# Optimization experiments

Hardware: AMD Instinct MI355X
Metric: run time of the kernel (lower is better)

## Reference

```python
import jax, jax.numpy as jnp
import numpy as np

NUM_SHOT = 1024
D_MODEL = 512
NHEAD = 8
NLAYERS = 6
D_FF = 2048
EPS = 1e-5


def _ln(x, s, b):
    m = jnp.mean(x, axis=-1, keepdims=True)
    v = jnp.mean(jnp.square(x - m), axis=-1, keepdims=True)
    return (x - m) / jnp.sqrt(v + EPS) * s + b


def _mha(q_in, kv_in, w_qkv, b_qkv, w_o, b_o):
    # q_in: [Sq, D], kv_in: [Sk, D]; PyTorch in_proj layout [3D, D]
    D = q_in.shape[-1]
    hd = D // NHEAD
    wq, wk, wv = w_qkv[:D], w_qkv[D:2 * D], w_qkv[2 * D:]
    bq, bk, bv = b_qkv[:D], b_qkv[D:2 * D], b_qkv[2 * D:]
    q = (q_in @ wq.T + bq).reshape(-1, NHEAD, hd)
    k = (kv_in @ wk.T + bk).reshape(-1, NHEAD, hd)
    v = (kv_in @ wv.T + bv).reshape(-1, NHEAD, hd)
    scores = jnp.einsum('qhd,khd->hqk', q, k) * (1.0 / np.sqrt(hd))
    a = jax.nn.softmax(scores, axis=-1)
    o = jnp.einsum('hqk,khd->qhd', a, v).reshape(-1, D)
    return o @ w_o.T + b_o


def setup_inputs() -> dict:
    key = jax.random.key(0)
    ks = iter(jax.random.split(key, 40))
    L, D, F = NLAYERS, D_MODEL, D_FF
    SC = 0.05  # weight scale, keeps activations sane

    def w(shape):
        return jax.random.normal(next(ks), shape, dtype=jnp.float32) * SC

    inp = {'shot_feature': jax.random.normal(next(ks), (NUM_SHOT, D), dtype=jnp.float32)}
    inp.update(
        enc_qkv_w=w((L, 3 * D, D)), enc_qkv_b=jnp.zeros((L, 3 * D), jnp.float32),
        enc_out_w=w((L, D, D)), enc_out_b=jnp.zeros((L, D), jnp.float32),
        enc_ff1_w=w((L, F, D)), enc_ff1_b=jnp.zeros((L, F), jnp.float32),
        enc_ff2_w=w((L, D, F)), enc_ff2_b=jnp.zeros((L, D), jnp.float32),
        enc_ln1_s=jnp.ones((L, D), jnp.float32), enc_ln1_b=jnp.zeros((L, D), jnp.float32),
        enc_ln2_s=jnp.ones((L, D), jnp.float32), enc_ln2_b=jnp.zeros((L, D), jnp.float32),
        dec_sa_qkv_w=w((L, 3 * D, D)), dec_sa_qkv_b=jnp.zeros((L, 3 * D), jnp.float32),
        dec_sa_out_w=w((L, D, D)), dec_sa_out_b=jnp.zeros((L, D), jnp.float32),
        dec_ca_qkv_w=w((L, 3 * D, D)), dec_ca_qkv_b=jnp.zeros((L, 3 * D), jnp.float32),
        dec_ca_out_w=w((L, D, D)), dec_ca_out_b=jnp.zeros((L, D), jnp.float32),
        dec_ff1_w=w((L, F, D)), dec_ff1_b=jnp.zeros((L, F), jnp.float32),
        dec_ff2_w=w((L, D, F)), dec_ff2_b=jnp.zeros((L, D), jnp.float32),
        dec_ln1_s=jnp.ones((L, D), jnp.float32), dec_ln1_b=jnp.zeros((L, D), jnp.float32),
        dec_ln2_s=jnp.ones((L, D), jnp.float32), dec_ln2_b=jnp.zeros((L, D), jnp.float32),
        dec_ln3_s=jnp.ones((L, D), jnp.float32), dec_ln3_b=jnp.zeros((L, D), jnp.float32),
        enc_norm_s=jnp.ones((D,), jnp.float32), enc_norm_b=jnp.zeros((D,), jnp.float32),
        dec_norm_s=jnp.ones((D,), jnp.float32), dec_norm_b=jnp.zeros((D,), jnp.float32),
    )
    return inp


def reference(shot_feature, enc_qkv_w, enc_qkv_b, enc_out_w, enc_out_b,
              enc_ff1_w, enc_ff1_b, enc_ff2_w, enc_ff2_b,
              enc_ln1_s, enc_ln1_b, enc_ln2_s, enc_ln2_b,
              dec_sa_qkv_w, dec_sa_qkv_b, dec_sa_out_w, dec_sa_out_b,
              dec_ca_qkv_w, dec_ca_qkv_b, dec_ca_out_w, dec_ca_out_b,
              dec_ff1_w, dec_ff1_b, dec_ff2_w, dec_ff2_b,
              dec_ln1_s, dec_ln1_b, dec_ln2_s, dec_ln2_b, dec_ln3_s, dec_ln3_b,
              enc_norm_s, enc_norm_b, dec_norm_s, dec_norm_b):
    x = shot_feature.reshape(NUM_SHOT, D_MODEL)  # batch dim of 1 squeezed

    # --- encoder (post-LN, ReLU FFN, dropout=eval identity) ---
    mem = x
    for i in range(NLAYERS):
        a = _mha(mem, mem, enc_qkv_w[i], enc_qkv_b[i], enc_out_w[i], enc_out_b[i])
        mem = _ln(mem + a, enc_ln1_s[i], enc_ln1_b[i])
        f = jax.nn.relu(mem @ enc_ff1_w[i].T + enc_ff1_b[i]) @ enc_ff2_w[i].T + enc_ff2_b[i]
        mem = _ln(mem + f, enc_ln2_s[i], enc_ln2_b[i])
    mem = _ln(mem, enc_norm_s, enc_norm_b)

    # --- decoder (tgt == src, no masks, matching original usage) ---
    y = x
    for i in range(NLAYERS):
        a = _mha(y, y, dec_sa_qkv_w[i], dec_sa_qkv_b[i], dec_sa_out_w[i], dec_sa_out_b[i])
        y = _ln(y + a, dec_ln1_s[i], dec_ln1_b[i])
        a = _mha(y, mem, dec_ca_qkv_w[i], dec_ca_qkv_b[i], dec_ca_out_w[i], dec_ca_out_b[i])
        y = _ln(y + a, dec_ln2_s[i], dec_ln2_b[i])
        f = jax.nn.relu(y @ dec_ff1_w[i].T + dec_ff1_b[i]) @ dec_ff2_w[i].T + dec_ff2_b[i]
        y = _ln(y + f, dec_ln3_s[i], dec_ln3_b[i])
    attention_out = _ln(y, dec_norm_s, dec_norm_b)  # [S, D]

    # --- fused pairwise cosine similarity (replaces O(n^2) python loop) ---
    n = attention_out / jnp.linalg.norm(attention_out, axis=1, keepdims=True)
    final_result = jax.lax.stop_gradient(n @ n.T)  # .detach() in original
    return (final_result, attention_out)
```

## Files before the change

### kernel.cpp

```cpp
#include <hip/hip_runtime.h>


#define NLAY 6

typedef __attribute__((ext_vector_type(8))) short short8;
typedef __attribute__((ext_vector_type(4))) short short4v;
typedef __attribute__((ext_vector_type(4))) float f32x4;

typedef __attribute__((address_space(3))) short lds_short;
typedef __attribute__((address_space(1))) const unsigned short g_ushort;

__device__ __forceinline__ void gload16(const unsigned short* g, short* l) {
    __builtin_amdgcn_global_load_lds((g_ushort*)g, (lds_short*)l, 16, 0, 0);
}

__device__ __forceinline__ void waitvm(int n) {
    if (n == 0)       asm volatile("s_waitcnt vmcnt(0)" ::: "memory");
    else if (n == 4)  asm volatile("s_waitcnt vmcnt(4)" ::: "memory");
    else if (n == 8)  asm volatile("s_waitcnt vmcnt(8)" ::: "memory");
    else              asm volatile("s_waitcnt vmcnt(16)" ::: "memory");
}

__device__ inline unsigned short f2bu(float x) {
    unsigned u = __builtin_bit_cast(unsigned, x);
    unsigned r = (u + 0x7fffu + ((u >> 16) & 1u)) >> 16;
    return (unsigned short)r;
}

__device__ inline float b2f(unsigned short u) {
    return __builtin_bit_cast(float, (unsigned)u << 16);
}

struct WCvt {
    const float* src[10];
    unsigned short* dst[10];
    long cum[11];
};

__global__ __launch_bounds__(256)
void f2ball_k(WCvt wc)
{
    const long total = wc.cum[10];
    for (long c = (long)blockIdx.x * 256 + threadIdx.x; c < total;
         c += (long)gridDim.x * 256) {
        int t = 0;
        #pragma unroll
        for (int i = 1; i < 10; ++i) if (c >= wc.cum[i]) t = i;
        const long o = (c - wc.cum[t]) * 8;
        const float* s = wc.src[t];
        unsigned short* d = wc.dst[t];
        const float4 a = *(const float4*)(s + o);
        const float4 b = *(const float4*)(s + o + 4);
        short8 v;
        v[0] = (short)f2bu(a.x); v[1] = (short)f2bu(a.y);
        v[2] = (short)f2bu(a.z); v[3] = (short)f2bu(a.w);
        v[4] = (short)f2bu(b.x); v[5] = (short)f2bu(b.y);
        v[6] = (short)f2bu(b.z); v[7] = (short)f2bu(b.w);
        *(short8*)(d + o) = v;
    }
}

__global__ __launch_bounds__(256)
void f2b_k(const float* __restrict__ s, unsigned short* __restrict__ d, long n)
{
    const long stride = (long)gridDim.x * 256;
    for (long i = (long)blockIdx.x * 256 + threadIdx.x; i * 8 < n; i += stride) {
        const long o = i * 8;
        const float4 a = *(const float4*)(s + o);
        const float4 b = *(const float4*)(s + o + 4);
        short8 v;
        v[0] = (short)f2bu(a.x); v[1] = (short)f2bu(a.y);
        v[2] = (short)f2bu(a.z); v[3] = (short)f2bu(a.w);
        v[4] = (short)f2bu(b.x); v[5] = (short)f2bu(b.y);
        v[6] = (short)f2bu(b.z); v[7] = (short)f2bu(b.w);
        *(short8*)(d + o) = v;
    }
}

template<bool RELU, bool OBF16>
__global__ __launch_bounds__(256)
void gemm3_k(const unsigned short* __restrict__ A,
             const unsigned short* __restrict__ A2, int a2_col, int lda,
             const unsigned short* __restrict__ B, int ldb,
             const float* __restrict__ bias,
             void* __restrict__ Cv, int ldc, long sC,
             int K, float alpha,
             unsigned short* __restrict__ VTp, int vt_col0, int kz,
             long zB, int zBias, long zVT)
{
    __shared__ __align__(16) short As[3][4096];
    __shared__ __align__(16) short Bs[3][4096];
    const int bz = blockIdx.z;
    const int m0 = blockIdx.y * 64;
    const int n0 = blockIdx.x * 64;
    if (A2 && n0 >= a2_col) A = A2;
    A += (long)bz * kz;
    B += (long)bz * kz + (long)bz * zB;
    if (bias) bias += (long)bz * zBias;
    if (VTp)  VTp  += (long)bz * zVT;
    const int tid = threadIdx.x;
    const int w  = tid >> 6;
    const int l  = tid & 63;
    const int fr = l & 15;
    const int kc = l >> 4;

    f32x4 acc[4] = {};
    const int T = K >> 6;

    auto FILL = [&](int t, int buf) {
        const int k0 = t * 64;
        #pragma unroll
        for (int it = 0; it < 2; ++it) {
            const int row = w * 16 + it * 8 + (l >> 3);
            const int sl  = ((l & 7) ^ (row & 7)) * 8;
            gload16(A + (long)(m0 + row) * lda + k0 + sl, &As[buf][(w * 16 + it * 8) * 64]);
            gload16(B + (long)(n0 + row) * ldb + k0 + sl, &Bs[buf][(w * 16 + it * 8) * 64]);
        }
    };

    FILL(0, 0);
    if (T > 1) FILL(1, 1);
    for (int t = 0; t < T; ++t) {
        waitvm(t + 1 < T ? 4 : 0);
        __builtin_amdgcn_sched_barrier(0);
        __builtin_amdgcn_s_barrier();
        if (t + 2 < T) FILL(t + 2, (t + 2) % 3);
        const int cb = t % 3;
        #pragma unroll
        for (int ks = 0; ks < 2; ++ks) {
            const int arow = w * 16 + fr;
            const short8 af = *(const short8*)&As[cb][arow * 64 + (((ks * 4 + kc) ^ (arow & 7)) * 8)];
            #pragma unroll
            for (int c = 0; c < 4; ++c) {
                const int brow = c * 16 + fr;
                const short8 bf = *(const short8*)&Bs[cb][brow * 64 + (((ks * 4 + kc) ^ (brow & 7)) * 8)];
                acc[c] = __builtin_amdgcn_mfma_f32_16x16x32_bf16(af, bf, acc[c], 0, 0, 0);
            }
        }
    }

    #pragma unroll
    for (int c = 0; c < 4; ++c) {
        const int n = n0 + c * 16 + fr;
        const float bv = bias ? bias[n] : 0.0f;
        #pragma unroll
        for (int i = 0; i < 4; ++i) {
            const long m = m0 + w * 16 + kc * 4 + i;
            float v = acc[c][i] * alpha + bv;
            if (RELU) v = fmaxf(v, 0.0f);
            if (OBF16) ((unsigned short*)Cv)[bz * sC + m * ldc + n] = f2bu(v);
            else       ((float*)Cv)[bz * sC + m * ldc + n] = v;
        }
    }

    if (VTp != nullptr && n0 >= vt_col0) {
        __syncthreads();
        short* TB = &As[0][0];
        #pragma unroll
        for (int c = 0; c < 4; ++c) {
            const int n = n0 + c * 16 + fr;
            const float bv = bias ? bias[n] : 0.0f;
            const int d = (n - vt_col0) & 63;
            #pragma unroll
            for (int i = 0; i < 4; ++i) {
                float v = acc[c][i] * alpha + bv;
                if (RELU) v = fmaxf(v, 0.0f);
                TB[d * 72 + w * 16 + kc * 4 + i] = (short)f2bu(v);
            }
        }
        __syncthreads();
        const long hh = (long)((n0 - vt_col0) >> 6);
        const int d  = tid >> 2;
        const int mc = (tid & 3) * 16;
        const short8 o0 = *(const short8*)&TB[d * 72 + mc];
        const short8 o1 = *(const short8*)&TB[d * 72 + mc + 8];
        unsigned short* dst = VTp + hh * 65536 + (long)d * 1024 + m0 + mc;
        *(short8*)dst = o0;
        *(short8*)(dst + 8) = o1;
    }
}

__global__ __launch_bounds__(128)
void attnp_k(const unsigned short* __restrict__ Qb, int qld,
             const unsigned short* __restrict__ Kb, int kld,
             const unsigned short* __restrict__ VT,
             const unsigned short* __restrict__ wo,
             unsigned short* __restrict__ SLABb)
{
    __shared__ __align__(16) short U[36928];
    short* Ks = U;
    short* Vs = U + 16384;
    short* Ps = U + 32768;
    float* Of = (float*)(U + 34816);
    float* Ml = (float*)(U + 34816 + 2048);
    const int qt = blockIdx.x;
    const int h  = blockIdx.y;
    const int tid = threadIdx.x;
    const int w  = tid >> 6;
    const int l  = tid & 63;
    const int fr = l & 15;
    const int kc = l >> 4;

    const int qrow = qt * 16 + fr;
    short8 qf[2];
    qf[0] = *(const short8*)(Qb + (long)qrow * qld + h * 64 + kc * 8);
    qf[1] = *(const short8*)(Qb + (long)qrow * qld + h * 64 + 32 + kc * 8);

    auto FILL = [&](int t, int lbuf) {
        const int kb  = (w * 8 + t) * 64;
        const int buf = w * 2 + lbuf;
        #pragma unroll
        for (int it = 0; it < 8; ++it) {
            const int row = it * 8 + (l >> 3);
            const int sl  = ((l & 7) ^ (row & 7)) * 8;
            gload16(Kb + (long)(kb + row) * kld + h * 64 + sl, Ks + buf * 4096 + it * 512);
            gload16(VT + (long)h * 65536 + (long)row * 1024 + kb + sl, Vs + buf * 4096 + it * 512);
        }
    };

    float m_i[4], l_i[4];
    f32x4 acc_o[4] = {};
    #pragma unroll
    for (int i = 0; i < 4; ++i) { m_i[i] = -1e30f; l_i[i] = 0.f; }

    short* ps = Ps + w * 1024;

    FILL(0, 0); FILL(1, 1);
    for (int t = 0; t < 8; ++t) {
        waitvm(t == 7 ? 0 : 16);
        __builtin_amdgcn_sched_barrier(0);
        const int cb = w * 2 + (t & 1);

        f32x4 sacc[4] = {};
        #pragma unroll
        for (int ks = 0; ks < 2; ++ks) {
            #pragma unroll
            for (int c = 0; c < 4; ++c) {
                const int krow = c * 16 + fr;
                const short8 kf = *(const short8*)(Ks + cb * 4096 + krow * 64 + (((ks * 4 + kc) ^ (krow & 7)) * 8));
                sacc[c] = __builtin_amdgcn_mfma_f32_16x16x32_bf16(qf[ks], kf, sacc[c], 0, 0, 0);
            }
        }

        float p[4][4];
        #pragma unroll
        for (int i = 0; i < 4; ++i) {
            float tm = fmaxf(fmaxf(sacc[0][i], sacc[1][i]), fmaxf(sacc[2][i], sacc[3][i]));
            #pragma unroll
            for (int off = 8; off; off >>= 1) tm = fmaxf(tm, __shfl_xor(tm, off));
            tm *= 0.125f;
            const float mn = fmaxf(m_i[i], tm);
            const float sc = __expf(m_i[i] - mn);
            m_i[i] = mn;
            float ts = 0.f;
            #pragma unroll
            for (int c = 0; c < 4; ++c) { p[c][i] = __expf(sacc[c][i] * 0.125f - mn); ts += p[c][i]; }
            #pragma unroll
            for (int off = 8; off; off >>= 1) ts += __shfl_xor(ts, off);
            l_i[i] = l_i[i] * sc + ts;
            #pragma unroll
            for (int c = 0; c < 4; ++c) acc_o[c][i] *= sc;
        }

        #pragma unroll
        for (int c = 0; c < 4; ++c) {
            const int col = c * 16 + fr;
            #pragma unroll
            for (int i = 0; i < 4; ++i) {
                const int row = kc * 4 + i;
                ps[row * 64 + (((col >> 3) ^ (row & 7)) * 8) + (col & 7)] = (short)f2bu(p[c][i]);
            }
        }
        short8 pf[2];
        pf[0] = *(const short8*)(ps + fr * 64 + ((kc ^ (fr & 7)) * 8));
        pf[1] = *(const short8*)(ps + fr * 64 + (((4 + kc) ^ (fr & 7)) * 8));

        #pragma unroll
        for (int ks = 0; ks < 2; ++ks) {
            #pragma unroll
            for (int c = 0; c < 4; ++c) {
                const int drow = c * 16 + fr;
                const short8 vf = *(const short8*)(Vs + cb * 4096 + drow * 64 + (((ks * 4 + kc) ^ (drow & 7)) * 8));
                acc_o[c] = __builtin_amdgcn_mfma_f32_16x16x32_bf16(pf[ks], vf, acc_o[c], 0, 0, 0);
            }
        }
        if (t + 2 < 8) FILL(t + 2, t & 1);
    }

    if (w == 1) {
        #pragma unroll
        for (int c = 0; c < 4; ++c)
            #pragma unroll
            for (int i = 0; i < 4; ++i)
                Of[(kc * 4 + i) * 64 + c * 16 + fr] = acc_o[c][i];
        if (fr == 0) {
            #pragma unroll
            for (int i = 0; i < 4; ++i) {
                Ml[(kc * 4 + i) * 2]     = m_i[i];
                Ml[(kc * 4 + i) * 2 + 1] = l_i[i];
            }
        }
    }
    __syncthreads();
    short* po = Ps;
    if (w == 0) {
        #pragma unroll
        for (int i = 0; i < 4; ++i) {
            const int row = kc * 4 + i;
            const float m1 = Ml[row * 2], l1 = Ml[row * 2 + 1];
            const float M  = fmaxf(m_i[i], m1);
            const float e0 = __expf(m_i[i] - M);
            const float e1 = __expf(m1 - M);
            const float inv = 1.0f / (e0 * l_i[i] + e1 * l1);
            #pragma unroll
            for (int c = 0; c < 4; ++c) {
                const int col = c * 16 + fr;
                const float o = e0 * acc_o[c][i] + e1 * Of[row * 64 + col];
                po[row * 64 + (((col >> 3) ^ (row & 7)) * 8) + (col & 7)] = (short)f2bu(o * inv);
            }
        }
    }
    __syncthreads();

    unsigned short* SLABh = SLABb + (long)h * 524288;
    auto WSTAGE = [&](int c8, int lbuf) {
        const int n0c = c8 * 64;
        const int buf = w * 2 + lbuf;
        #pragma unroll
        for (int it = 0; it < 8; ++it) {
            const int row = it * 8 + (l >> 3);
            const int sl  = ((l & 7) ^ (row & 7)) * 8;
            gload16(wo + (long)(n0c + row) * 512 + h * 64 + sl, Ks + buf * 4096 + it * 512);
        }
    };

    WSTAGE(w * 4, 0);
    for (int j = 0; j < 4; ++j) {
        if (j + 1 < 4) WSTAGE(w * 4 + j + 1, (j + 1) & 1);
        waitvm(j + 1 < 4 ? 8 : 0);
        __builtin_amdgcn_sched_barrier(0);
        const int buf = w * 2 + (j & 1);
        f32x4 a2[4] = {};
        #pragma unroll
        for (int ks = 0; ks < 2; ++ks) {
            const int q = ks * 4 + kc;
            const short8 af = *(const short8*)(po + fr * 64 + ((q ^ (fr & 7)) * 8));
            #pragma unroll
            for (int ct = 0; ct < 4; ++ct) {
                const int brn = ct * 16 + fr;
                const short8 bf = *(const short8*)(Ks + buf * 4096 + brn * 64 + ((q ^ (brn & 7)) * 8));
                a2[ct] = __builtin_amdgcn_mfma_f32_16x16x32_bf16(af, bf, a2[ct], 0, 0, 0);
            }
        }
        const int c8 = w * 4 + j;
        #pragma unroll
        for (int ct = 0; ct < 4; ++ct) {
            const int n = c8 * 64 + ct * 16 + fr;
            #pragma unroll
            for (int i = 0; i < 4; ++i)
                SLABh[(long)(qt * 16 + kc * 4 + i) * 512 + n] = f2bu(a2[ct][i]);
        }
    }
}

template<int NSLAB, bool SB16, int FIN>
__global__ __launch_bounds__(256)
void ln_k(const float* __restrict__ x, const void* __restrict__ slab,
          const float* __restrict__ bias,
          const float* __restrict__ s, const float* __restrict__ b,
          float* __restrict__ outf, unsigned short* __restrict__ outb,
          const float* __restrict__ s2, const float* __restrict__ b2,
          float* __restrict__ oattn, unsigned short* __restrict__ nbb)
{
    const int lane = threadIdx.x & 63;
    const int row  = (blockIdx.x << 2) + (threadIdx.x >> 6);
    const float* px = x + (long)row * 512;
    float v[8];
    float sum = 0.f;
    #pragma unroll
    for (int i = 0; i < 8; ++i) {
        const int j = lane + (i << 6);
        v[i] = px[j];
        #pragma unroll
        for (int t = 0; t < NSLAB; ++t) {
            if (SB16) v[i] += b2f(((const unsigned short*)slab)[(long)t * 524288 + (long)row * 512 + j]);
            else      v[i] += ((const float*)slab)[(long)t * 524288 + (long)row * 512 + j];
        }
        if (NSLAB > 0) v[i] += bias[j];
        sum += v[i];
    }
    #pragma unroll
    for (int off = 32; off; off >>= 1) sum += __shfl_xor(sum, off);
    const float m = sum * (1.0f / 512.0f);
    float s2v = 0.f;
    #pragma unroll
    for (int i = 0; i < 8; ++i) { const float d = v[i] - m; s2v += d * d; }
    #pragma unroll
    for (int off = 32; off; off >>= 1) s2v += __shfl_xor(s2v, off);
    const float inv = rsqrtf(s2v * (1.0f / 512.0f) + 1e-5f);
    float r[8];
    #pragma unroll
    for (int i = 0; i < 8; ++i) {
        const int j = lane + (i << 6);
        r[i] = (v[i] - m) * inv * s[j] + b[j];
    }
    if (FIN == 0) {
        #pragma unroll
        for (int i = 0; i < 8; ++i) {
            const int j = lane + (i << 6);
            outf[(long)row * 512 + j] = r[i];
            outb[(long)row * 512 + j] = f2bu(r[i]);
        }
    } else {
        float sum2 = 0.f;
        #pragma unroll
        for (int i = 0; i < 8; ++i) sum2 += r[i];
        #pragma unroll
        for (int off = 32; off; off >>= 1) sum2 += __shfl_xor(sum2, off);
        const float m2 = sum2 * (1.0f / 512.0f);
        float q2 = 0.f;
        #pragma unroll
        for (int i = 0; i < 8; ++i) { const float d = r[i] - m2; q2 += d * d; }
        #pragma unroll
        for (int off = 32; off; off >>= 1) q2 += __shfl_xor(q2, off);
        const float inv2 = rsqrtf(q2 * (1.0f / 512.0f) + 1e-5f);
        if (FIN == 1) {
            #pragma unroll
            for (int i = 0; i < 8; ++i) {
                const int j = lane + (i << 6);
                outb[(long)row * 512 + j] = f2bu((r[i] - m2) * inv2 * s2[j] + b2[j]);
            }
        } else {
            float r2[8];
            float nrm = 0.f;
            #pragma unroll
            for (int i = 0; i < 8; ++i) {
                const int j = lane + (i << 6);
                r2[i] = (r[i] - m2) * inv2 * s2[j] + b2[j];
                oattn[(long)row * 512 + j] = r2[i];
                nrm += r2[i] * r2[i];
            }
            #pragma unroll
            for (int off = 32; off; off >>= 1) nrm += __shfl_xor(nrm, off);
            const float rinv = rsqrtf(nrm);
            #pragma unroll
            for (int i = 0; i < 8; ++i)
                nbb[(long)row * 512 + lane + (i << 6)] = f2bu(r2[i] * rinv);
        }
    }
}

__global__ __launch_bounds__(256)
void init_k(const float* __restrict__ x, float* __restrict__ mf, float* __restrict__ yf,
            unsigned short* __restrict__ mb, unsigned short* __restrict__ yb)
{
    const long i = ((long)blockIdx.x * 256 + threadIdx.x) * 4;
    const float4 v = *(const float4*)(x + i);
    *(float4*)(mf + i) = v;
    *(float4*)(yf + i) = v;
    short4v s;
    s[0] = (short)f2bu(v.x); s[1] = (short)f2bu(v.y);
    s[2] = (short)f2bu(v.z); s[3] = (short)f2bu(v.w);
    *(short4v*)(mb + i) = s;
    *(short4v*)(yb + i) = s;
}

static void gemm3(hipStream_t st, bool relu, bool obf16,
                  const unsigned short* A, int lda,
                  const unsigned short* B, int ldb,
                  const float* bias, void* C, int ldc, long sC,
                  int M, int N, int K, float alpha, int batch,
                  unsigned short* VTp = nullptr, int vt_col0 = 0,
                  const unsigned short* A2 = nullptr, int a2_col = 0,
                  int kz = 0, long zB = 0, int zBias = 0, long zVT = 0)
{
    dim3 g(N / 64, M / 64, batch);
    if (obf16) {
        if (relu) gemm3_k<true,  true ><<<g, 256, 0, st>>>(A, A2, a2_col, lda, B, ldb, bias, C, ldc, sC, K, alpha, VTp, vt_col0, kz, zB, zBias, zVT);
        else      gemm3_k<false, true ><<<g, 256, 0, st>>>(A, A2, a2_col, lda, B, ldb, bias, C, ldc, sC, K, alpha, VTp, vt_col0, kz, zB, zBias, zVT);
    } else {
        if (relu) gemm3_k<true,  false><<<g, 256, 0, st>>>(A, A2, a2_col, lda, B, ldb, bias, C, ldc, sC, K, alpha, VTp, vt_col0, kz, zB, zBias, zVT);
        else      gemm3_k<false, false><<<g, 256, 0, st>>>(A, A2, a2_col, lda, B, ldb, bias, C, ldc, sC, K, alpha, VTp, vt_col0, kz, zB, zBias, zVT);
    }
}

extern "C" void kernel_launch(void* const* d_in, const int* in_sizes, int n_in,
                              void* d_out, int out_size, void* d_ws, size_t ws_size,
                              hipStream_t stream)
{
    const float* x            = (const float*)d_in[0];
    const float* enc_qkv_w    = (const float*)d_in[1];
    const float* enc_qkv_b    = (const float*)d_in[2];
    const float* enc_out_w    = (const float*)d_in[3];
    const float* enc_out_b    = (const float*)d_in[4];
    const float* enc_ff1_w    = (const float*)d_in[5];
    const float* enc_ff1_b    = (const float*)d_in[6];
    const float* enc_ff2_w    = (const float*)d_in[7];
    const float* enc_ff2_b    = (const float*)d_in[8];
    const float* enc_ln1_s    = (const float*)d_in[9];
    const float* enc_ln1_b    = (const float*)d_in[10];
    const float* enc_ln2_s    = (const float*)d_in[11];
    const float* enc_ln2_b    = (const float*)d_in[12];
    const float* dec_sa_qkv_w = (const float*)d_in[13];
    const float* dec_sa_qkv_b = (const float*)d_in[14];
    const float* dec_sa_out_w = (const float*)d_in[15];
    const float* dec_sa_out_b = (const float*)d_in[16];
    const float* dec_ca_qkv_w = (const float*)d_in[17];
    const float* dec_ca_qkv_b = (const float*)d_in[18];
    const float* dec_ca_out_w = (const float*)d_in[19];
    const float* dec_ca_out_b = (const float*)d_in[20];
    const float* dec_ff1_w    = (const float*)d_in[21];
    const float* dec_ff1_b    = (const float*)d_in[22];
    const float* dec_ff2_w    = (const float*)d_in[23];
    const float* dec_ff2_b    = (const float*)d_in[24];
    const float* dec_ln1_s    = (const float*)d_in[25];
    const float* dec_ln1_b    = (const float*)d_in[26];
    const float* dec_ln2_s    = (const float*)d_in[27];
    const float* dec_ln2_b    = (const float*)d_in[28];
    const float* dec_ln3_s    = (const float*)d_in[29];
    const float* dec_ln3_b    = (const float*)d_in[30];
    const float* enc_norm_s   = (const float*)d_in[31];
    const float* enc_norm_b   = (const float*)d_in[32];
    const float* dec_norm_s   = (const float*)d_in[33];
    const float* dec_norm_b   = (const float*)d_in[34];

    char* p = (char*)d_ws;
    auto alloc = [&](size_t bytes) -> char* {
        char* r = p; p += (bytes + 255) & ~(size_t)255; return r;
    };
    float*          MEMf = (float*)alloc(1024 * 512 * 4);
    float*          Yf   = (float*)alloc(1024 * 512 * 4);
    unsigned short* MEMb = (unsigned short*)alloc(1024 * 512 * 2);
    unsigned short* Yb   = (unsigned short*)alloc(1024 * 512 * 2);
    unsigned short* QKVb = (unsigned short*)alloc(1024 * 1536 * 2);
    unsigned short* VT   = (unsigned short*)alloc(8L * 64 * 1024 * 2);
    char*           SLAB = alloc(8L * 1024 * 512 * 2);
    unsigned short* F1b  = (unsigned short*)alloc(1024L * 2048 * 2);
    unsigned short* NBb  = (unsigned short*)alloc(1024 * 512 * 2);
    unsigned short* QB   = (unsigned short*)alloc(1024 * 512 * 2);
    unsigned short* KVCA = (unsigned short*)alloc(6L * 1024 * 1024 * 2);
    unsigned short* VTCA = (unsigned short*)alloc(6L * 8 * 64 * 1024 * 2);

    const float* wsrc[10] = {enc_qkv_w, enc_out_w, enc_ff1_w, enc_ff2_w,
                             dec_sa_qkv_w, dec_sa_out_w, dec_ca_qkv_w, dec_ca_out_w,
                             dec_ff1_w, dec_ff2_w};
    const long wper[10] = {1536L*512, 512L*512, 2048L*512, 512L*2048,
                           1536L*512, 512L*512, 1536L*512, 512L*512,
                           2048L*512, 512L*2048};
    long wtot = 0;
    for (int t = 0; t < 10; ++t) wtot += wper[t] * NLAY;

    const size_t used = (size_t)(p - (char*)d_ws);
    const bool preconv = (ws_size > used) && ((ws_size - used) >= (size_t)wtot * 2 + 4096);

    unsigned short* wpre[10] = {};
    unsigned short* slots[2] = {};
    int slot_ctr = 0;
    if (preconv) {
        WCvt wc;
        wc.cum[0] = 0;
        for (int t = 0; t < 10; ++t) {
            wpre[t] = (unsigned short*)alloc((size_t)wper[t] * NLAY * 2);
            wc.src[t] = wsrc[t];
            wc.dst[t] = wpre[t];
            wc.cum[t + 1] = wc.cum[t] + wper[t] * NLAY / 8;
        }
        f2ball_k<<<dim3(2048), 256, 0, stream>>>(wc);
    } else {
        slots[0] = (unsigned short*)alloc(2048L * 512 * 2);
        slots[1] = (unsigned short*)alloc(2048L * 512 * 2);
    }
    auto W = [&](int t, int layer) -> const unsigned short* {
        if (preconv) return wpre[t] + (long)layer * wper[t];
        unsigned short* dst = slots[(slot_ctr++) & 1];
        const long n = wper[t];
        long blocks = (n / 8 + 255) / 256; if (blocks > 2048) blocks = 2048;
        f2b_k<<<dim3((unsigned)blocks), 256, 0, stream>>>(wsrc[t] + (long)layer * wper[t], dst, n);
        return dst;
    };

    float* out_gram = (float*)d_out;
    float* out_attn = out_gram + 1024 * 1024;

    auto run_self = [&](const unsigned short* xb_in, int wt_qkv, int wt_o, int layer,
                        const float* bqkv, const float* obias,
                        const float* lns, const float* lnb,
                        float* xf, unsigned short* xb) {
        gemm3(stream, false, true, xb_in, 512, W(wt_qkv, layer), 512, bqkv,
              QKVb, 1536, 0, 1024, 1536, 512, 1.0f, 1, VT, 1024);
        attnp_k<<<dim3(64, 8), 128, 0, stream>>>(QKVb, 1536, QKVb + 512, 1536, VT,
                                                 W(wt_o, layer), (unsigned short*)SLAB);
        ln_k<8, true, 0><<<256, 256, 0, stream>>>(xf, SLAB, obias, lns, lnb, xf, xb,
                                                  nullptr, nullptr, nullptr, nullptr);
    };
    auto run_ffn = [&](unsigned short* inb, int wt1, int wt2, int layer,
                       const float* b1, const float* f2bias,
                       const float* lns, const float* lnb,
                       float* xf, unsigned short* xb, int fin,
                       const float* s2, const float* b2) {
        gemm3(stream, true, true, inb, 512, W(wt1, layer), 512, b1,
              F1b, 2048, 0, 1024, 2048, 512, 1.0f, 1);
        gemm3(stream, false, true, F1b, 2048, W(wt2, layer), 2048, nullptr,
              SLAB, 512, 524288, 1024, 512, 512, 1.0f, 4, nullptr, 0, nullptr, 0, 512);
        if (fin == 0)
            ln_k<4, true, 0><<<256, 256, 0, stream>>>(xf, SLAB, f2bias, lns, lnb, xf, xb,
                                                      nullptr, nullptr, nullptr, nullptr);
        else if (fin == 1)
            ln_k<4, true, 1><<<256, 256, 0, stream>>>(xf, SLAB, f2bias, lns, lnb, xf, xb,
                                                      s2, b2, nullptr, nullptr);
        else
            ln_k<4, true, 2><<<256, 256, 0, stream>>>(xf, SLAB, f2bias, lns, lnb, xf, xb,
                                                      s2, b2, out_attn, NBb);
    };

    init_k<<<512, 256, 0, stream>>>(x, MEMf, Yf, MEMb, Yb);

    for (int i = 0; i < NLAY; ++i) {
        run_self(MEMb, 0, 1, i, enc_qkv_b + i * 1536, enc_out_b + i * 512,
                 enc_ln1_s + i * 512, enc_ln1_b + i * 512, MEMf, MEMb);
        run_ffn(MEMb, 2, 3, i, enc_ff1_b + i * 2048, enc_ff2_b + i * 512,
                enc_ln2_s + i * 512, enc_ln2_b + i * 512, MEMf, MEMb,
                (i == NLAY - 1) ? 1 : 0, enc_norm_s, enc_norm_b);
    }

    if (preconv) {
        gemm3(stream, false, true, MEMb, 512, wpre[6] + 512L * 512, 512,
              dec_ca_qkv_b + 512, KVCA, 1024, 1024L * 1024,
              1024, 1024, 512, 1.0f, 6, VTCA, 512,
              nullptr, 0, 0, 1536L * 512, 1536, 524288L);
    }

    for (int i = 0; i < NLAY; ++i) {
        run_self(Yb, 4, 5, i, dec_sa_qkv_b + i * 1536, dec_sa_out_b + i * 512,
                 dec_ln1_s + i * 512, dec_ln1_b + i * 512, Yf, Yb);

        if (preconv) {
            gemm3(stream, false, true, Yb, 512, W(6, i), 512, dec_ca_qkv_b + i * 1536,
                  QB, 512, 0, 1024, 512, 512, 1.0f, 1);
            attnp_k<<<dim3(64, 8), 128, 0, stream>>>(QB, 512,
                    KVCA + (long)i * 1024 * 1024, 1024, VTCA + (long)i * 524288,
                    W(7, i), (unsigned short*)SLAB);
        } else {
            gemm3(stream, false, true, Yb, 512, W(6, i), 512, dec_ca_qkv_b + i * 1536,
                  QKVb, 1536, 0, 1024, 1536, 512, 1.0f, 1, VT, 1024, MEMb, 512);
            attnp_k<<<dim3(64, 8), 128, 0, stream>>>(QKVb, 1536, QKVb + 512, 1536, VT,
                                                     W(7, i), (unsigned short*)SLAB);
        }
        ln_k<8, true, 0><<<256, 256, 0, stream>>>(Yf, SLAB, dec_ca_out_b + i * 512,
                                                  dec_ln2_s + i * 512, dec_ln2_b + i * 512,
                                                  Yf, Yb, nullptr, nullptr, nullptr, nullptr);

        run_ffn(Yb, 8, 9, i, dec_ff1_b + i * 2048, dec_ff2_b + i * 512,
                dec_ln3_s + i * 512, dec_ln3_b + i * 512, Yf, Yb,
                (i == NLAY - 1) ? 2 : 0, dec_norm_s, dec_norm_b);
    }

    gemm3(stream, false, false, NBb, 512, NBb, 512, nullptr,
          out_gram, 1024, 0, 1024, 1024, 512, 1.0f, 1);
}
```

Before: 960.1 us.

## Fuse post-attention LayerNorm into attention kernel via last-block atomic counter

Each attention block bumps a per-query-tile atomic counter after writing its per-head slab. The last of the 8 head blocks then sums the slabs, adds the residual and bias, and applies LayerNorm itself, which removes a separate ln_k launch per attention. The input copy/convert (init_k) is also folded into the weight-conversion kernel, saving another launch. The cost is that the reduction runs serially in one 128-thread block per tile, and correctness now depends on fences and counter resets.

After: 1.577 ms. 64.3% more time.

```diff
diff --git a/kernel.cpp b/kernel.cpp
--- a/kernel.cpp
+++ b/kernel.cpp
@@ -35,14 +35,36 @@
     const float* src[10];
     unsigned short* dst[10];
     long cum[11];
+    const float* x;
+    float* mf; float* yf;
+    unsigned short* mb; unsigned short* yb;
+    int* cnt;
 };
 
 __global__ __launch_bounds__(256)
 void f2ball_k(WCvt wc)
 {
-    const long total = wc.cum[10];
+    if (blockIdx.x == 0 && threadIdx.x < 64)
+        __hip_atomic_store(&wc.cnt[threadIdx.x], 0, __ATOMIC_RELAXED, __HIP_MEMORY_SCOPE_AGENT);
+    const long wtot  = wc.cum[10];
+    const long total = wtot + 65536;
     for (long c = (long)blockIdx.x * 256 + threadIdx.x; c < total;
          c += (long)gridDim.x * 256) {
+        if (c >= wtot) {
+            const long o = (c - wtot) * 8;
+            const float4 a = *(const float4*)(wc.x + o);
+            const float4 b = *(const float4*)(wc.x + o + 4);
+            *(float4*)(wc.mf + o) = a;  *(float4*)(wc.mf + o + 4) = b;
+            *(float4*)(wc.yf + o) = a;  *(float4*)(wc.yf + o + 4) = b;
+            short8 v;
+            v[0] = (short)f2bu(a.x); v[1] = (short)f2bu(a.y);
+            v[2] = (short)f2bu(a.z); v[3] = (short)f2bu(a.w);
+            v[4] = (short)f2bu(b.x); v[5] = (short)f2bu(b.y);
+            v[6] = (short)f2bu(b.z); v[7] = (short)f2bu(b.w);
+            *(short8*)(wc.mb + o) = v;
+            *(short8*)(wc.yb + o) = v;
+            continue;
+        }
         int t = 0;
         #pragma unroll
         for (int i = 1; i < 10; ++i) if (c >= wc.cum[i]) t = i;
@@ -185,9 +207,14 @@
              const unsigned short* __restrict__ Kb, int kld,
              const unsigned short* __restrict__ VT,
              const unsigned short* __restrict__ wo,
-             unsigned short* __restrict__ SLABb)
+             unsigned short* __restrict__ SLABb,
+             const float* __restrict__ xf_in, const float* __restrict__ obias,
+             const float* __restrict__ lns, const float* __restrict__ lnb,
+             float* __restrict__ xf_out, unsigned short* __restrict__ xb_out,
+             int* __restrict__ cnt)
 {
     __shared__ __align__(16) short U[36928];
+    __shared__ int lastflag;
     short* Ks = U;
     short* Vs = U + 16384;
     short* Ps = U + 32768;
@@ -359,6 +386,53 @@
             #pragma unroll
             for (int i = 0; i < 4; ++i)
                 SLABh[(long)(qt * 16 + kc * 4 + i) * 512 + n] = f2bu(a2[ct][i]);
+        }
+    }
+
+    __syncthreads();
+    if (tid == 0) {
+        __threadfence();
+        const int old = __hip_atomic_fetch_add(&cnt[qt], 1,
+                          __ATOMIC_ACQ_REL, __HIP_MEMORY_SCOPE_AGENT);
+        lastflag = (old == 7) ? 1 : 0;
+        if (lastflag) {
+            __hip_atomic_store(&cnt[qt], 0, __ATOMIC_RELAXED, __HIP_MEMORY_SCOPE_AGENT);
+            __threadfence();
+        }
+    }
+    __syncthreads();
+    if (!lastflag) return;
+
+    for (int it = 0; it < 8; ++it) {
+        const int row = qt * 16 + w * 8 + it;
+        const long base = (long)row * 512;
+        float v[8];
+        float sum = 0.f;
+        #pragma unroll
+        for (int i = 0; i < 8; ++i) {
+            const int j = l + (i << 6);
+            v[i] = xf_in[base + j];
+            #pragma unroll
+            for (int t = 0; t < 8; ++t)
+                v[i] += b2f(SLABb[(long)t * 524288 + base + j]);
+            v[i] += obias[j];
+            sum += v[i];
+        }
+        #pragma unroll
+        for (int off = 32; off; off >>= 1) sum += __shfl_xor(sum, off);
+        const float mn = sum * (1.0f / 512.0f);
+        float q = 0.f;
+        #pragma unroll
+        for (int i = 0; i < 8; ++i) { const float d = v[i] - mn; q += d * d; }
+        #pragma unroll
+        for (int off = 32; off; off >>= 1) q += __shfl_xor(q, off);
+        const float inv = rsqrtf(q * (1.0f / 512.0f) + 1e-5f);
+        #pragma unroll
+        for (int i = 0; i < 8; ++i) {
+            const int j = l + (i << 6);
+            const float r = (v[i] - mn) * inv * lns[j] + lnb[j];
+            xf_out[base + j] = r;
+            xb_out[base + j] = f2bu(r);
         }
     }
 }
@@ -452,8 +526,11 @@
 
 __global__ __launch_bounds__(256)
 void init_k(const float* __restrict__ x, float* __restrict__ mf, float* __restrict__ yf,
-            unsigned short* __restrict__ mb, unsigned short* __restrict__ yb)
+            unsigned short* __restrict__ mb, unsigned short* __restrict__ yb,
+            int* __restrict__ cnt)
 {
+    if (blockIdx.x == 0 && threadIdx.x < 64)
+        __hip_atomic_store(&cnt[threadIdx.x], 0, __ATOMIC_RELAXED, __HIP_MEMORY_SCOPE_AGENT);
     const long i = ((long)blockIdx.x * 256 + threadIdx.x) * 4;
     const float4 v = *(const float4*)(x + i);
     *(float4*)(mf + i) = v;
@@ -528,6 +605,7 @@
     auto alloc = [&](size_t bytes) -> char* {
         char* r = p; p += (bytes + 255) & ~(size_t)255; return r;
     };
+    int*            CNT  = (int*)alloc(64 * 4);
     float*          MEMf = (float*)alloc(1024 * 512 * 4);
     float*          Yf   = (float*)alloc(1024 * 512 * 4);
     unsigned short* MEMb = (unsigned short*)alloc(1024 * 512 * 2);
@@ -565,10 +643,12 @@
             wc.dst[t] = wpre[t];
             wc.cum[t + 1] = wc.cum[t] + wper[t] * NLAY / 8;
         }
+        wc.x = x; wc.mf = MEMf; wc.yf = Yf; wc.mb = MEMb; wc.yb = Yb; wc.cnt = CNT;
         f2ball_k<<<dim3(2048), 256, 0, stream>>>(wc);
     } else {
         slots[0] = (unsigned short*)alloc(2048L * 512 * 2);
         slots[1] = (unsigned short*)alloc(2048L * 512 * 2);
+        init_k<<<512, 256, 0, stream>>>(x, MEMf, Yf, MEMb, Yb, CNT);
     }
     auto W = [&](int t, int layer) -> const unsigned short* {
         if (preconv) return wpre[t] + (long)layer * wper[t];
@@ -589,9 +669,8 @@
         gemm3(stream, false, true, xb_in, 512, W(wt_qkv, layer), 512, bqkv,
               QKVb, 1536, 0, 1024, 1536, 512, 1.0f, 1, VT, 1024);
         attnp_k<<<dim3(64, 8), 128, 0, stream>>>(QKVb, 1536, QKVb + 512, 1536, VT,
-                                                 W(wt_o, layer), (unsigned short*)SLAB);
-        ln_k<8, true, 0><<<256, 256, 0, stream>>>(xf, SLAB, obias, lns, lnb, xf, xb,
-                                                  nullptr, nullptr, nullptr, nullptr);
+                W(wt_o, layer), (unsigned short*)SLAB,
+                xf, obias, lns, lnb, xf, xb, CNT);
     };
     auto run_ffn = [&](unsigned short* inb, int wt1, int wt2, int layer,
                        const float* b1, const float* f2bias,
@@ -613,8 +692,6 @@
                                                       s2, b2, out_attn, NBb);
     };
 
-    init_k<<<512, 256, 0, stream>>>(x, MEMf, Yf, MEMb, Yb);
-
     for (int i = 0; i < NLAY; ++i) {
         run_self(MEMb, 0, 1, i, enc_qkv_b + i * 1536, enc_out_b + i * 512,
                  enc_ln1_s + i * 512, enc_ln1_b + i * 512, MEMf, MEMb);
@@ -639,16 +716,17 @@
                   QB, 512, 0, 1024, 512, 512, 1.0f, 1);
             attnp_k<<<dim3(64, 8), 128, 0, stream>>>(QB, 512,
                     KVCA + (long)i * 1024 * 1024, 1024, VTCA + (long)i * 524288,
-                    W(7, i), (unsigned short*)SLAB);
+                    W(7, i), (unsigned short*)SLAB,
+                    Yf, dec_ca_out_b + i * 512, dec_ln2_s + i * 512, dec_ln2_b + i * 512,
+                    Yf, Yb, CNT);
         } else {
             gemm3(stream, false, true, Yb, 512, W(6, i), 512, dec_ca_qkv_b + i * 1536,
                   QKVb, 1536, 0, 1024, 1536, 512, 1.0f, 1, VT, 1024, MEMb, 512);
             attnp_k<<<dim3(64, 8), 128, 0, stream>>>(QKVb, 1536, QKVb + 512, 1536, VT,
-                                                     W(7, i), (unsigned short*)SLAB);
-        }
-        ln_k<8, true, 0><<<256, 256, 0, stream>>>(Yf, SLAB, dec_ca_out_b + i * 512,
-                                                  dec_ln2_s + i * 512, dec_ln2_b + i * 512,
-                                                  Yf, Yb, nullptr, nullptr, nullptr, nullptr);
+                    W(7, i), (unsigned short*)SLAB,
+                    Yf, dec_ca_out_b + i * 512, dec_ln2_s + i * 512, dec_ln2_b + i * 512,
+                    Yf, Yb, CNT);
+        }
 
         run_ffn(Yb, 8, 9, i, dec_ff1_b + i * 2048, dec_ff2_b + i * 512,
                 dec_ln3_s + i * 512, dec_ln3_b + i * 512, Yf, Yb,
```
